# Kernel optimization log

Hardware: AMD Instinct MI355X
Metric: run time of the kernel (lower is better)

The kernel has to match this reference:

```python
import jax, jax.numpy as jnp
import numpy as np

EPS = 1e-6

def _grad_magnitude(x):
    # x: [B, 1, D, H, W]. Valid 3x3x3 conv with shift-subtract kernels:
    # kernel_w differences along D, kernel_d along H, kernel_h along W.
    g_w = x[:, :, 2:, 1:-1, 1:-1] - x[:, :, :-2, 1:-1, 1:-1]
    g_d = x[:, :, 1:-1, 2:, 1:-1] - x[:, :, 1:-1, :-2, 1:-1]
    g_h = x[:, :, 1:-1, 1:-1, 2:] - x[:, :, 1:-1, 1:-1, :-2]
    mag = jnp.sqrt(g_w * g_w + g_d * g_d + g_h * g_h + EPS)
    # replicate-pad back to original spatial size
    return jnp.pad(mag, ((0, 0), (0, 0), (1, 1), (1, 1), (1, 1)), mode='edge')

def setup_inputs() -> dict:
    key = jax.random.key(0)
    k1, k2 = jax.random.split(key)
    shape = (1, 1, 256, 256, 256)
    x1 = jax.random.normal(k1, shape, dtype=jnp.float32)
    x2 = jax.random.normal(k2, shape, dtype=jnp.float32)
    return {"x1": x1, "x2": x2}

def reference(x1, x2):
    g1 = _grad_magnitude(x1)
    g2 = _grad_magnitude(x2)
    return jnp.mean(jnp.abs(g1 - g2))
```

## Files before the change

kernel.cpp:

```cpp
#include <hip/hip_runtime.h>


__global__ void init_acc_kernel(double* __restrict__ acc) {
    acc[threadIdx.x] = 0.0;
}

__global__ __launch_bounds__(256) void grad_loss_kernel(const float4* __restrict__ x1,
                                                        const float4* __restrict__ x2,
                                                        double* __restrict__ acc) {
    const int tid   = threadIdx.x;
    const int lane  = tid & 63;
    const int hslot = tid >> 6;
    const int htile = blockIdx.x & 63;
    const int dchk  = blockIdx.x >> 6;

    const int h  = 1 + htile * 4 + hslot;
    const int d0 = 1 + dchk * 16;

    float ww0, ww1, ww2, ww3;
    {
        const int wbase = 4 * lane;
        ww0 = (wbase + 0 == 0)   ? 0.0f : ((wbase + 0 == 1)   ? 2.0f : 1.0f);
        ww1 = (wbase + 1 == 1)   ? 2.0f : 1.0f;
        ww2 = (wbase + 2 == 254) ? 2.0f : 1.0f;
        ww3 = (wbase + 3 == 255) ? 0.0f : ((wbase + 3 == 254) ? 2.0f : 1.0f);
    }

    float val = 0.0f;

    if (h <= 254) {
        const float whf = (h == 1 || h == 254) ? 2.0f : 1.0f;
        const int rowbase = h * 64 + lane;

        float4 a1 = x1[(d0 - 1) * 16384 + rowbase];
        float4 b1 = x1[d0 * 16384 + rowbase];
        float4 a2 = x2[(d0 - 1) * 16384 + rowbase];
        float4 b2 = x2[d0 * 16384 + rowbase];

        const int dend = (d0 + 16 <= 255) ? (d0 + 16) : 255;
        for (int d = d0; d < dend; ++d) {
            const int base = d * 16384 + rowbase;
            float4 c1 = x1[base + 16384];
            float4 u1 = x1[base - 64];
            float4 v1 = x1[base + 64];
            float4 c2 = x2[base + 16384];
            float4 u2 = x2[base - 64];
            float4 v2 = x2[base + 64];

            float l1 = __shfl_up(b1.w, 1, 64);
            float r1 = __shfl_down(b1.x, 1, 64);
            float l2 = __shfl_up(b2.w, 1, 64);
            float r2 = __shfl_down(b2.x, 1, 64);

            float gw, gd, gh, m10, m11, m12, m13, m20, m21, m22, m23;

            gw = c1.x - a1.x; gd = v1.x - u1.x; gh = b1.y - l1;
            m10 = sqrtf(gw * gw + gd * gd + gh * gh + 1e-6f);
            gw = c1.y - a1.y; gd = v1.y - u1.y; gh = b1.z - b1.x;
            m11 = sqrtf(gw * gw + gd * gd + gh * gh + 1e-6f);
            gw = c1.z - a1.z; gd = v1.z - u1.z; gh = b1.w - b1.y;
            m12 = sqrtf(gw * gw + gd * gd + gh * gh + 1e-6f);
            gw = c1.w - a1.w; gd = v1.w - u1.w; gh = r1 - b1.z;
            m13 = sqrtf(gw * gw + gd * gd + gh * gh + 1e-6f);

            gw = c2.x - a2.x; gd = v2.x - u2.x; gh = b2.y - l2;
            m20 = sqrtf(gw * gw + gd * gd + gh * gh + 1e-6f);
            gw = c2.y - a2.y; gd = v2.y - u2.y; gh = b2.z - b2.x;
            m21 = sqrtf(gw * gw + gd * gd + gh * gh + 1e-6f);
            gw = c2.z - a2.z; gd = v2.z - u2.z; gh = b2.w - b2.y;
            m22 = sqrtf(gw * gw + gd * gd + gh * gh + 1e-6f);
            gw = c2.w - a2.w; gd = v2.w - u2.w; gh = r2 - b2.z;
            m23 = sqrtf(gw * gw + gd * gd + gh * gh + 1e-6f);

            float inner = ww0 * fabsf(m10 - m20)
                        + ww1 * fabsf(m11 - m21)
                        + ww2 * fabsf(m12 - m22)
                        + ww3 * fabsf(m13 - m23);

            const float wdf = (d == 1 || d == 254) ? 2.0f : 1.0f;
            val += wdf * whf * inner;

            a1 = b1; b1 = c1;
            a2 = b2; b2 = c2;
        }
    }

    for (int off = 32; off > 0; off >>= 1)
        val += __shfl_down(val, off, 64);

    __shared__ float smem[4];
    const int lid = tid & 63;
    const int wid = tid >> 6;
    if (lid == 0) smem[wid] = val;
    __syncthreads();

    if (wid == 0) {
        float s = (lid < 4) ? smem[lid] : 0.0f;
        s += __shfl_down(s, 2, 64);
        s += __shfl_down(s, 1, 64);
        if (lid == 0)
            atomicAdd(&acc[blockIdx.x & 255], (double)s);
    }
}

__global__ void finalize_kernel(const double* __restrict__ acc, float* __restrict__ out) {
    double v = acc[threadIdx.x];
    for (int off = 32; off > 0; off >>= 1)
        v += __shfl_down(v, off, 64);

    __shared__ double smem[4];
    const int lid = threadIdx.x & 63;
    const int wid = threadIdx.x >> 6;
    if (lid == 0) smem[wid] = v;
    __syncthreads();

    if (threadIdx.x == 0) {
        double s = smem[0] + smem[1] + smem[2] + smem[3];
        out[0] = (float)(s / 16777216.0);
    }
}

extern "C" void kernel_launch(void* const* d_in, const int* in_sizes, int n_in,
                              void* d_out, int out_size, void* d_ws, size_t ws_size,
                              hipStream_t stream) {
    const float4* x1 = (const float4*)d_in[0];
    const float4* x2 = (const float4*)d_in[1];
    float* out = (float*)d_out;
    double* acc = (double*)d_ws;

    init_acc_kernel<<<1, 256, 0, stream>>>(acc);
    grad_loss_kernel<<<64 * 16, 256, 0, stream>>>(x1, x2, acc);
    finalize_kernel<<<1, 256, 0, stream>>>(acc, out);
}
```

Baseline: 157.4 us.

## Shrink depth chunks to raise block count and fuse finalize via last-block ticket

Cuts the per-block depth chunk from 16 to 4 slices, quadrupling the grid to 4096 blocks for more parallelism across CUs. The finalize kernel is folded into the main kernel with a ticket counter so the last block reduces the accumulators, and the init kernel becomes a memset. Smaller chunks add halo reloads (two extra slices per four), raising memory traffic, and more blocks mean more atomics on the accumulators.

```diff
diff --git a/kernel.cpp b/kernel.cpp
--- a/kernel.cpp
+++ b/kernel.cpp
@@ -1,13 +1,13 @@
 #include <hip/hip_runtime.h>
 
 
-__global__ void init_acc_kernel(double* __restrict__ acc) {
-    acc[threadIdx.x] = 0.0;
-}
+#define NBLOCKS (64 * 64)
 
 __global__ __launch_bounds__(256) void grad_loss_kernel(const float4* __restrict__ x1,
                                                         const float4* __restrict__ x2,
-                                                        double* __restrict__ acc) {
+                                                        double* __restrict__ acc,
+                                                        unsigned int* __restrict__ ticket,
+                                                        float* __restrict__ out) {
     const int tid   = threadIdx.x;
     const int lane  = tid & 63;
     const int hslot = tid >> 6;
@@ -15,7 +15,7 @@
     const int dchk  = blockIdx.x >> 6;
 
     const int h  = 1 + htile * 4 + hslot;
-    const int d0 = 1 + dchk * 16;
+    const int d0 = 1 + dchk * 4;
 
     float ww0, ww1, ww2, ww3;
     {
@@ -37,7 +37,7 @@
         float4 a2 = x2[(d0 - 1) * 16384 + rowbase];
         float4 b2 = x2[d0 * 16384 + rowbase];
 
-        const int dend = (d0 + 16 <= 255) ? (d0 + 16) : 255;
+        const int dend = (d0 + 4 <= 255) ? (d0 + 4) : 255;
         for (int d = d0; d < dend; ++d) {
             const int base = d * 16384 + rowbase;
             float4 c1 = x1[base + 16384];
@@ -89,34 +89,32 @@
         val += __shfl_down(val, off, 64);
 
     __shared__ float smem[4];
+    __shared__ int is_last;
     const int lid = tid & 63;
     const int wid = tid >> 6;
     if (lid == 0) smem[wid] = val;
     __syncthreads();
 
-    if (wid == 0) {
-        float s = (lid < 4) ? smem[lid] : 0.0f;
-        s += __shfl_down(s, 2, 64);
-        s += __shfl_down(s, 1, 64);
-        if (lid == 0)
-            atomicAdd(&acc[blockIdx.x & 255], (double)s);
+    if (tid == 0) {
+        float s = smem[0] + smem[1] + smem[2] + smem[3];
+        atomicAdd(&acc[blockIdx.x & 255], (double)s);
+        __threadfence();
+        unsigned int old = atomicAdd(ticket, 1u);
+        is_last = (old == NBLOCKS - 1) ? 1 : 0;
     }
-}
-
-__global__ void finalize_kernel(const double* __restrict__ acc, float* __restrict__ out) {
-    double v = acc[threadIdx.x];
-    for (int off = 32; off > 0; off >>= 1)
-        v += __shfl_down(v, off, 64);
-
-    __shared__ double smem[4];
-    const int lid = threadIdx.x & 63;
-    const int wid = threadIdx.x >> 6;
-    if (lid == 0) smem[wid] = v;
     __syncthreads();
 
-    if (threadIdx.x == 0) {
-        double s = smem[0] + smem[1] + smem[2] + smem[3];
-        out[0] = (float)(s / 16777216.0);
+    if (is_last) {
+        double v = atomicAdd(&acc[tid], 0.0);
+        for (int off = 32; off > 0; off >>= 1)
+            v += __shfl_down(v, off, 64);
+        __shared__ double dmem[4];
+        if (lid == 0) dmem[wid] = v;
+        __syncthreads();
+        if (tid == 0) {
+            double s = dmem[0] + dmem[1] + dmem[2] + dmem[3];
+            out[0] = (float)(s / 16777216.0);
+        }
     }
 }
 
@@ -127,8 +125,8 @@
     const float4* x2 = (const float4*)d_in[1];
     float* out = (float*)d_out;
     double* acc = (double*)d_ws;
+    unsigned int* ticket = (unsigned int*)(acc + 256);
 
-    init_acc_kernel<<<1, 256, 0, stream>>>(acc);
-    grad_loss_kernel<<<64 * 16, 256, 0, stream>>>(x1, x2, acc);
-    finalize_kernel<<<1, 256, 0, stream>>>(acc, out);
+    hipMemsetAsync(d_ws, 0, 256 * sizeof(double) + 64, stream);
+    grad_loss_kernel<<<NBLOCKS, 256, 0, stream>>>(x1, x2, acc, ticket, out);
 }
```

After: 316.3 us. 2.01x slower.
